# Kernel optimization log

Measured on AMD Instinct MI355X. Metric: run time of the kernel, lower is better.

The kernel has to match this reference:

```python
import jax, jax.numpy as jnp
import numpy as np

B, N, I, D, K = 64, 16, 2048, 32, 32  # batch, num_capsule, input_num_capsule, dim_capsule, input_dim_capsule
ROUTINGS = 3
EPS = 1e-07


def squash(s):
    # squared_norm includes per-element eps before the sum, matching torch code
    sq = jnp.sum(s * s + EPS, axis=-1, keepdims=True)
    return sq * s / ((1.0 + sq) * jnp.sqrt(sq))


def setup_inputs() -> dict:
    key = jax.random.key(0)
    kx, kw = jax.random.split(key)
    x = jax.random.normal(kx, (B, I, K), dtype=jnp.float32)
    # xavier_uniform over a [N, I, D, K] tensor: fan_in = D*K (last two dims treated as matrix by torch init? torch treats dim1.. as fan) -- use gain=1 uniform bound per torch's convention: fan_in = I*D*K/... Use simple xavier over (fan_in=K, fan_out=D) receptive field I*N.
    fan_in = I * K
    fan_out = I * D  # torch: fan_in = size(1)*receptive, here just use uniform bound from full-tensor xavier
    bound = float(np.sqrt(6.0 / (fan_in + fan_out)))
    W = jax.random.uniform(kw, (N, I, D, K), minval=-bound, maxval=bound, dtype=jnp.float32)
    return {"x": x, "W": W}


def reference(x, W):
    # u_hat[b,n,i,d] = sum_k W[n,i,d,k] * x[b,i,k]
    u_hat = jnp.einsum('nidk,bik->bnid', W, x)
    b = jnp.zeros((B, N, I), dtype=u_hat.dtype)
    v = None
    for r in range(ROUTINGS):
        c = jax.nn.softmax(b, axis=1)                 # softmax over num_capsule
        s = jnp.einsum('bni,bnid->bnd', c, u_hat)     # [B, N, D]
        v = squash(s)
        if r < ROUTINGS - 1:
            a = jnp.einsum('bnid,bnd->bni', u_hat, v)
            b = b + a
    return v  # [B, N, D]
```

## Files before the change

### kernel.cpp

```cpp
#include <hip/hip_runtime.h>
#include <stdint.h>

#define Bdim 64
#define Ndim 16
#define Idim 2048
#define Ddim 32
#define Kdim 32
#define EPSV 1e-7f

#define TILE_I   4
#define TILES_PB 16
#define NB_Y     (Idim / (TILE_I * TILES_PB))

typedef __attribute__((ext_vector_type(8))) short short8v;
typedef __attribute__((ext_vector_type(4))) float f32x4;

static __device__ __forceinline__ unsigned pk_rne(float a, float b) {
    unsigned ua = __float_as_uint(a);
    unsigned ub = __float_as_uint(b);
    ua = (ua + 0x7fffu + ((ua >> 16) & 1u)) >> 16;
    ub = (ub + 0x7fffu + ((ub >> 16) & 1u)) >> 16;
    return (ua & 0xffffu) | (ub << 16);
}
static __device__ __forceinline__ float bf2f(unsigned us) {
    return __uint_as_float(us << 16);
}

#define GLL16(g, s)                                                              \
    __builtin_amdgcn_global_load_lds(                                            \
        (const __attribute__((address_space(1))) void*)(uintptr_t)(const void*)(g), \
        (__attribute__((address_space(3))) void*)(uintptr_t)(void*)(s), 16, 0, 0)

__global__ __launch_bounds__(256) void convert_x(
    const float* __restrict__ x, unsigned short* __restrict__ x2)
{
    const int i  = blockIdx.x;
    const int b  = threadIdx.x >> 2;
    const int ko = threadIdx.x & 3;
    const float* src = x + ((size_t)b * Idim + i) * Kdim + (ko << 3);
    float4 a = ((const float4*)src)[0];
    float4 c = ((const float4*)src)[1];
    uint4 o;
    o.x = pk_rne(a.x, a.y); o.y = pk_rne(a.z, a.w);
    o.z = pk_rne(c.x, c.y); o.w = pk_rne(c.z, c.w);
    *(uint4*)(x2 + ((size_t)i * 64 + b) * 32 + (ko << 3)) = o;
}

__global__ __launch_bounds__(256) void pass1_dma(
    const float* __restrict__ W, const unsigned short* __restrict__ x2,
    unsigned short* __restrict__ uhat, float* __restrict__ s0)
{
    __shared__ float          ldsW[2][TILE_I * 1024];
    __shared__ unsigned short ldsX[2][TILE_I * 2048];

    const int n     = blockIdx.x;
    const int iblk0 = blockIdx.y * (TILE_I * TILES_PB);
    const int tid   = threadIdx.x;
    const int l     = tid & 63;
    const int bcol  = ((tid >> 6) << 4) + (l & 15);
    const int krow  = l >> 4;

    const float*          Wblk = W  + ((size_t)n * Idim + iblk0) * (Ddim * Kdim);
    const unsigned short* Xblk = x2 + (size_t)iblk0 * (64 * 32);

    f32x4 acc0 = {0.f, 0.f, 0.f, 0.f};
    f32x4 acc1 = {0.f, 0.f, 0.f, 0.f};
    const f32x4 zero = {0.f, 0.f, 0.f, 0.f};

    auto stage = [&](int t, int buf) {
        const float* Wt = Wblk + (size_t)t * (TILE_I * 1024);
        float* dw = &ldsW[buf][0];
        #pragma unroll
        for (int j = 0; j < 4; ++j) {
            const int c  = j * 256 + tid;
            const int lc = c & 63, h = (c >> 6) & 1, mt = (c >> 7) & 1, il = c >> 8;
            const float* src = Wt + il * 1024 + ((mt << 4) + (lc & 15)) * 32
                                  + ((lc >> 4) << 3) + (h << 2);
            GLL16(src, dw + (size_t)c * 4);
        }
        const unsigned short* Xt = Xblk + (size_t)t * (TILE_I * 2048);
        unsigned short* dx = &ldsX[buf][0];
        #pragma unroll
        for (int j = 0; j < 4; ++j) {
            const int c = j * 256 + tid;
            GLL16(Xt + (size_t)c * 8, dx + (size_t)c * 8);
        }
    };

    stage(0, 0);

    for (int t = 0; t < TILES_PB; ++t) {
        if (t + 1 < TILES_PB) stage(t + 1, (t + 1) & 1);
        asm volatile("s_waitcnt vmcnt(8)" ::: "memory");
        __builtin_amdgcn_s_barrier();
        __builtin_amdgcn_sched_barrier(0);

        const float*          lw = &ldsW[t & 1][0];
        const unsigned short* lx = &ldsX[t & 1][0];
        const int ibase = iblk0 + t * TILE_I;

        #pragma unroll
        for (int il = 0; il < TILE_I; ++il) {
            const int i = ibase + il;

            union { short8v v; unsigned u[4]; } bf, af0, af1;
            bf.v = *(const short8v*)(lx + il * 2048 + bcol * 32 + (krow << 3));

            const float4 w00 = *(const float4*)(lw + ((il * 256 + l)       << 2));
            const float4 w01 = *(const float4*)(lw + ((il * 256 + 64 + l)  << 2));
            const float4 w10 = *(const float4*)(lw + ((il * 256 + 128 + l) << 2));
            const float4 w11 = *(const float4*)(lw + ((il * 256 + 192 + l) << 2));
            af0.u[0] = pk_rne(w00.x, w00.y); af0.u[1] = pk_rne(w00.z, w00.w);
            af0.u[2] = pk_rne(w01.x, w01.y); af0.u[3] = pk_rne(w01.z, w01.w);
            af1.u[0] = pk_rne(w10.x, w10.y); af1.u[1] = pk_rne(w10.z, w10.w);
            af1.u[2] = pk_rne(w11.x, w11.y); af1.u[3] = pk_rne(w11.z, w11.w);

            f32x4 c0 = __builtin_amdgcn_mfma_f32_16x16x32_bf16(af0.v, bf.v, zero, 0, 0, 0);
            f32x4 c1 = __builtin_amdgcn_mfma_f32_16x16x32_bf16(af1.v, bf.v, zero, 0, 0, 0);

            const size_t ubase = (((size_t)bcol * Idim + i) * Ndim + n) * Ddim + (krow << 2);
            uint2 p0; p0.x = pk_rne(c0[0], c0[1]); p0.y = pk_rne(c0[2], c0[3]);
            *(uint2*)(uhat + ubase) = p0;
            uint2 p1; p1.x = pk_rne(c1[0], c1[1]); p1.y = pk_rne(c1[2], c1[3]);
            *(uint2*)(uhat + ubase + 16) = p1;

            acc0 += c0;
            acc1 += c1;
        }
        asm volatile("s_waitcnt lgkmcnt(0)" ::: "memory");
        __builtin_amdgcn_s_barrier();
        __builtin_amdgcn_sched_barrier(0);
    }

    float* sp = s0 + ((size_t)bcol * Ndim + n) * Ddim + (krow << 2);
    #pragma unroll
    for (int r = 0; r < 4; ++r) atomicAdd(sp + r, acc0[r]);
    #pragma unroll
    for (int r = 0; r < 4; ++r) atomicAdd(sp + 16 + r, acc1[r]);
}

__global__ __launch_bounds__(256) void pass1_simple(
    const float* __restrict__ W, const float* __restrict__ x,
    unsigned short* __restrict__ uhat, float* __restrict__ s0, int bbase)
{
    const int IB = 16;
    const int n  = blockIdx.x;
    const int i0 = blockIdx.y * IB;
    const int w  = threadIdx.x >> 6;
    const int l  = threadIdx.x & 63;
    const int bcol  = (w << 4) + (l & 15);
    const int bglob = bbase + bcol;
    const int krow  = l >> 4;

    f32x4 acc0 = {0.f,0.f,0.f,0.f}, acc1 = {0.f,0.f,0.f,0.f};
    const f32x4 zero = {0.f,0.f,0.f,0.f};

    for (int ii = 0; ii < IB; ++ii) {
        const int i = i0 + ii;
        const float* xp = x + ((size_t)bglob * Idim + i) * Kdim + (krow << 3);
        float4 xa = ((const float4*)xp)[0];
        float4 xb = ((const float4*)xp)[1];
        union { short8v v; unsigned u[4]; } bf, af0, af1;
        bf.u[0]=pk_rne(xa.x,xa.y); bf.u[1]=pk_rne(xa.z,xa.w);
        bf.u[2]=pk_rne(xb.x,xb.y); bf.u[3]=pk_rne(xb.z,xb.w);

        const float* wbase = W + ((size_t)n * Idim + i) * Ddim * Kdim + (krow << 3);
        const float* wp0 = wbase + (size_t)(l & 15) * Kdim;
        float4 wa = ((const float4*)wp0)[0];
        float4 wb = ((const float4*)wp0)[1];
        af0.u[0]=pk_rne(wa.x,wa.y); af0.u[1]=pk_rne(wa.z,wa.w);
        af0.u[2]=pk_rne(wb.x,wb.y); af0.u[3]=pk_rne(wb.z,wb.w);
        const float* wp1 = wp0 + 16 * Kdim;
        float4 wc = ((const float4*)wp1)[0];
        float4 wd = ((const float4*)wp1)[1];
        af1.u[0]=pk_rne(wc.x,wc.y); af1.u[1]=pk_rne(wc.z,wc.w);
        af1.u[2]=pk_rne(wd.x,wd.y); af1.u[3]=pk_rne(wd.z,wd.w);

        f32x4 c0 = __builtin_amdgcn_mfma_f32_16x16x32_bf16(af0.v, bf.v, zero, 0,0,0);
        f32x4 c1 = __builtin_amdgcn_mfma_f32_16x16x32_bf16(af1.v, bf.v, zero, 0,0,0);

        const size_t ubase = (((size_t)bcol * Idim + i) * Ndim + n) * Ddim + (krow << 2);
        uint2 p0; p0.x=pk_rne(c0[0],c0[1]); p0.y=pk_rne(c0[2],c0[3]);
        *(uint2*)(uhat + ubase) = p0;
        uint2 p1; p1.x=pk_rne(c1[0],c1[1]); p1.y=pk_rne(c1[2],c1[3]);
        *(uint2*)(uhat + ubase + 16) = p1;
        acc0 += c0; acc1 += c1;
    }
    float* sp = s0 + ((size_t)bglob * Ndim + n) * Ddim + (krow << 2);
    #pragma unroll
    for (int r = 0; r < 4; ++r) atomicAdd(sp + r, acc0[r]);
    #pragma unroll
    for (int r = 0; r < 4; ++r) atomicAdd(sp + 16 + r, acc1[r]);
}

template<int FIRST>
__global__ __launch_bounds__(256) void route_kernel(
    const unsigned short* __restrict__ uhat, const float* __restrict__ vin,
    float* __restrict__ bbuf, float* __restrict__ sout, int bbase)
{
    const int bc = blockIdx.x;
    const int it = blockIdx.y;
    const int w = threadIdx.x >> 6;
    const int l = threadIdx.x & 63;
    const int g = l >> 2, q = l & 3;
    const int bglob = bbase + bc;

    const float* vp = vin + ((size_t)bglob * Ndim + g) * Ddim + (q << 3);
    float vreg[8];
    *(float4*)&vreg[0] = ((const float4*)vp)[0];
    *(float4*)&vreg[4] = ((const float4*)vp)[1];

    float sacc[8];
    #pragma unroll
    for (int j = 0; j < 8; ++j) sacc[j] = 0.f;

    for (int ii = w; ii < 128; ii += 4) {
        const int i = (it << 7) + ii;
        const unsigned short* up = uhat + ((size_t)bc * Idim + i) * (Ndim * Ddim) + (l << 3);
        uint4 uraw = *(const uint4*)up;
        float u[8];
        u[0] = bf2f(uraw.x & 0xffffu); u[1] = bf2f(uraw.x >> 16);
        u[2] = bf2f(uraw.y & 0xffffu); u[3] = bf2f(uraw.y >> 16);
        u[4] = bf2f(uraw.z & 0xffffu); u[5] = bf2f(uraw.z >> 16);
        u[6] = bf2f(uraw.w & 0xffffu); u[7] = bf2f(uraw.w >> 16);

        float p = 0.f;
        #pragma unroll
        for (int j = 0; j < 8; ++j) p = fmaf(u[j], vreg[j], p);
        p += __shfl_xor(p, 1);
        p += __shfl_xor(p, 2);

        float logit = p;
        if (FIRST) {
            if (q == 0) bbuf[((size_t)bc * Idim + i) * Ndim + g] = p;
        } else {
            logit += bbuf[((size_t)bc * Idim + i) * Ndim + g];
        }
        float m = logit;
        m = fmaxf(m, __shfl_xor(m, 4));
        m = fmaxf(m, __shfl_xor(m, 8));
        m = fmaxf(m, __shfl_xor(m, 16));
        m = fmaxf(m, __shfl_xor(m, 32));
        float e = __expf(logit - m);
        float z = e;
        z += __shfl_xor(z, 4);
        z += __shfl_xor(z, 8);
        z += __shfl_xor(z, 16);
        z += __shfl_xor(z, 32);
        float c = e / z;

        #pragma unroll
        for (int j = 0; j < 8; ++j) sacc[j] = fmaf(c, u[j], sacc[j]);
    }

    __shared__ float sl[4][512];
    #pragma unroll
    for (int j = 0; j < 8; ++j) sl[w][(l << 3) + j] = sacc[j];
    __syncthreads();
    for (int e2 = threadIdx.x; e2 < 512; e2 += 256) {
        float vsum = sl[0][e2] + sl[1][e2] + sl[2][e2] + sl[3][e2];
        atomicAdd(sout + (size_t)bglob * (Ndim * Ddim) + e2, vsum);
    }
}

__global__ __launch_bounds__(256) void squash_kernel(
    const float* __restrict__ s, float* __restrict__ vout, float scale, int bbase)
{
    const int tid = blockIdx.x * 256 + threadIdx.x;
    const int row = tid >> 5;
    const int d   = tid & 31;
    const size_t off = ((size_t)bbase * Ndim + row) * Ddim + d;
    float sv = s[off] * scale;
    float t = fmaf(sv, sv, EPSV);
    t += __shfl_xor(t, 1);
    t += __shfl_xor(t, 2);
    t += __shfl_xor(t, 4);
    t += __shfl_xor(t, 8);
    t += __shfl_xor(t, 16);
    float vv = sv * t / ((1.f + t) * sqrtf(t));
    vout[off] = vv;
}

extern "C" void kernel_launch(void* const* d_in, const int* in_sizes, int n_in,
                              void* d_out, int out_size, void* d_ws, size_t ws_size,
                              hipStream_t stream)
{
    (void)in_sizes; (void)n_in; (void)out_size;
    const float* x = (const float*)d_in[0];
    const float* W = (const float*)d_in[1];
    float* out = (float*)d_out;

    const size_t snd = (size_t)Bdim * Ndim * Ddim;
    const size_t fixed = 5 * snd * sizeof(float);

    int Bc = 64;
    while (Bc > 16) {
        size_t need = (size_t)Bc * Idim * Ndim * Ddim * 2 + (size_t)Bc * Idim * Ndim * 4 + fixed;
        if (need <= ws_size) break;
        Bc >>= 1;
    }

    char* p = (char*)d_ws;
    unsigned short* uhat = (unsigned short*)p; p += (size_t)Bc * Idim * Ndim * Ddim * 2;
    float* bbuf = (float*)p;                   p += (size_t)Bc * Idim * Ndim * 4;
    float* sbuf = (float*)p;
    float* s0 = sbuf;
    float* s1 = sbuf + snd;
    float* s2 = sbuf + 2 * snd;
    float* v0 = sbuf + 3 * snd;
    float* v1 = sbuf + 4 * snd;

    for (int bbase = 0; bbase < Bdim; bbase += Bc) {
        (void)hipMemsetAsync(sbuf, 0, 3 * snd * sizeof(float), stream);

        if (Bc == 64) {
            unsigned short* x2 = (unsigned short*)bbuf;
            convert_x<<<dim3(Idim), 256, 0, stream>>>(x, x2);
            pass1_dma<<<dim3(Ndim, NB_Y), 256, 0, stream>>>(W, x2, uhat, s0);
        } else {
            pass1_simple<<<dim3(Ndim, Idim / 16), dim3(64 * (Bc / 16)), 0, stream>>>(
                W, x, uhat, s0, bbase);
        }
        squash_kernel<<<dim3(Bc * 2), 256, 0, stream>>>(s0, v0, 1.f / 16.f, bbase);

        route_kernel<1><<<dim3(Bc, Idim / 128), 256, 0, stream>>>(uhat, v0, bbuf, s1, bbase);
        squash_kernel<<<dim3(Bc * 2), 256, 0, stream>>>(s1, v1, 1.f, bbase);

        route_kernel<0><<<dim3(Bc, Idim / 128), 256, 0, stream>>>(uhat, v1, bbuf, s2, bbase);
        squash_kernel<<<dim3(Bc * 2), 256, 0, stream>>>(s2, out, 1.f, bbase);
    }
}
```

Before: 171.3 us.

## Stage W and x tiles as contiguous padded LDS chunks with halved I-tile

Replaces the scattered per-thread global_load_lds addressing with contiguous 1KB chunk loads per wave into padded LDS chunks (stride 1056). The MFMA fragment reads are re-indexed to match. TILE_I drops from 4 to 2, which halves LDS per buffer and doubles the number of blocks along I. The waitcnt counts are adjusted because each stage now issues fewer loads. The aim is coalesced global reads and fewer LDS bank conflicts, at the cost of more blocks and a more intricate read pattern.

```diff
diff --git a/kernel.cpp b/kernel.cpp
--- a/kernel.cpp
+++ b/kernel.cpp
@@ -8,9 +8,11 @@
 #define Kdim 32
 #define EPSV 1e-7f
 
-#define TILE_I   4
-#define TILES_PB 16
-#define NB_Y     (Idim / (TILE_I * TILES_PB))
+#define TILE_I    2
+#define TILES_PB  16
+#define NB_Y      (Idim / (TILE_I * TILES_PB))
+#define CSTRIDE   1056
+#define NCHUNK    16
 
 typedef __attribute__((ext_vector_type(8))) short short8v;
 typedef __attribute__((ext_vector_type(4))) float f32x4;
@@ -50,14 +52,14 @@
     const float* __restrict__ W, const unsigned short* __restrict__ x2,
     unsigned short* __restrict__ uhat, float* __restrict__ s0)
 {
-    __shared__ float          ldsW[2][TILE_I * 1024];
-    __shared__ unsigned short ldsX[2][TILE_I * 2048];
+    __shared__ char lds[2][NCHUNK * CSTRIDE];
 
     const int n     = blockIdx.x;
     const int iblk0 = blockIdx.y * (TILE_I * TILES_PB);
     const int tid   = threadIdx.x;
     const int l     = tid & 63;
-    const int bcol  = ((tid >> 6) << 4) + (l & 15);
+    const int wv    = tid >> 6;
+    const int bcol  = (wv << 4) + (l & 15);
     const int krow  = l >> 4;
 
     const float*          Wblk = W  + ((size_t)n * Idim + iblk0) * (Ddim * Kdim);
@@ -68,22 +70,21 @@
     const f32x4 zero = {0.f, 0.f, 0.f, 0.f};
 
     auto stage = [&](int t, int buf) {
-        const float* Wt = Wblk + (size_t)t * (TILE_I * 1024);
-        float* dw = &ldsW[buf][0];
+        char* base = &lds[buf][0];
+        const float*          Wt = Wblk + (size_t)t * (TILE_I * 1024);
+        const unsigned short* Xt = Xblk + (size_t)t * (TILE_I * 2048);
         #pragma unroll
         for (int j = 0; j < 4; ++j) {
-            const int c  = j * 256 + tid;
-            const int lc = c & 63, h = (c >> 6) & 1, mt = (c >> 7) & 1, il = c >> 8;
-            const float* src = Wt + il * 1024 + ((mt << 4) + (lc & 15)) * 32
-                                  + ((lc >> 4) << 3) + (h << 2);
-            GLL16(src, dw + (size_t)c * 4);
-        }
-        const unsigned short* Xt = Xblk + (size_t)t * (TILE_I * 2048);
-        unsigned short* dx = &ldsX[buf][0];
-        #pragma unroll
-        for (int j = 0; j < 4; ++j) {
-            const int c = j * 256 + tid;
-            GLL16(Xt + (size_t)c * 8, dx + (size_t)c * 8);
+            const int g = j * 4 + wv;
+            char* dst = base + g * CSTRIDE;
+            if (g < 8) {
+                const float* src = Wt + ((g >> 2) * 1024 + (g & 3) * 256) + (l << 2);
+                GLL16(src, dst);
+            } else {
+                const int p = g - 8;
+                const unsigned short* src = Xt + ((p >> 2) * 2048 + (p & 3) * 512) + (l << 3);
+                GLL16(src, dst);
+            }
         }
     };
 
@@ -91,12 +92,15 @@
 
     for (int t = 0; t < TILES_PB; ++t) {
         if (t + 1 < TILES_PB) stage(t + 1, (t + 1) & 1);
-        asm volatile("s_waitcnt vmcnt(8)" ::: "memory");
+        if (t == 0 || t == TILES_PB - 1) {
+            asm volatile("s_waitcnt vmcnt(4)" ::: "memory");
+        } else {
+            asm volatile("s_waitcnt vmcnt(8)" ::: "memory");
+        }
         __builtin_amdgcn_s_barrier();
         __builtin_amdgcn_sched_barrier(0);
 
-        const float*          lw = &ldsW[t & 1][0];
-        const unsigned short* lx = &ldsX[t & 1][0];
+        const char* base = &lds[t & 1][0];
         const int ibase = iblk0 + t * TILE_I;
 
         #pragma unroll
@@ -104,12 +108,16 @@
             const int i = ibase + il;
 
             union { short8v v; unsigned u[4]; } bf, af0, af1;
-            bf.v = *(const short8v*)(lx + il * 2048 + bcol * 32 + (krow << 3));
-
-            const float4 w00 = *(const float4*)(lw + ((il * 256 + l)       << 2));
-            const float4 w01 = *(const float4*)(lw + ((il * 256 + 64 + l)  << 2));
-            const float4 w10 = *(const float4*)(lw + ((il * 256 + 128 + l) << 2));
-            const float4 w11 = *(const float4*)(lw + ((il * 256 + 192 + l) << 2));
+            bf.v = *(const short8v*)(base + (8 + il * 4 + wv) * CSTRIDE
+                                          + ((l & 15) << 6) + ((l >> 4) << 4));
+
+            const int wrow = ((l & 7) << 7) + ((l >> 4) << 5);
+            const char* wc0 = base + (il * 4 + 0 + ((l >> 3) & 1)) * CSTRIDE + wrow;
+            const char* wc1 = base + (il * 4 + 2 + ((l >> 3) & 1)) * CSTRIDE + wrow;
+            const float4 w00 = *(const float4*)(wc0);
+            const float4 w01 = *(const float4*)(wc0 + 16);
+            const float4 w10 = *(const float4*)(wc1);
+            const float4 w11 = *(const float4*)(wc1 + 16);
             af0.u[0] = pk_rne(w00.x, w00.y); af0.u[1] = pk_rne(w00.z, w00.w);
             af0.u[2] = pk_rne(w01.x, w01.y); af0.u[3] = pk_rne(w01.z, w01.w);
             af1.u[0] = pk_rne(w10.x, w10.y); af1.u[1] = pk_rne(w10.z, w10.w);
```

New measurement: 194.2 us. +13.4%, slower.
